# Optimization experiments

Hardware: AMD Instinct MI355X
Metric: run time of the kernel (lower is better)

## Reference

```python
import jax, jax.numpy as jnp
import numpy as np

N = 8192          # batch size (anchors == candidates, self-mining)
D = 128           # embedding dim
NUM_CLASSES = 256 # label vocabulary
MAX_K = 64        # static cap on negatives sampled per row (k ~= class_count-1 ~ 31)
MIN_DIST = 0.1
MAX_DIST = 1.42


def setup_inputs() -> dict:
    key = jax.random.key(0)
    k1, k2 = jax.random.split(key)
    l_embeds = jax.random.normal(k1, (N, D), dtype=jnp.float32)
    l_labels = jax.random.randint(k2, (N,), 0, NUM_CLASSES)
    return {"l_embeds": l_embeds, "l_labels": l_labels}


def reference(l_embeds, l_labels):
    # --- Miner.forward: L2-normalize embeddings (normalize_embeds=True) ---
    x = l_embeds / jnp.linalg.norm(l_embeds, axis=1, keepdims=True)

    # --- cdist(x, x, p=2) via gram matrix ---
    sq = jnp.sum(x * x, axis=1)                      # [N]
    d2 = sq[:, None] + sq[None, :] - 2.0 * (x @ x.T)  # [N, N]
    dist = jnp.sqrt(jnp.clip(d2, 0.0))

    # Exclude self-pairs: original adds inf on the diagonal; setting the diagonal
    # to MAX_DIST achieves the intended effect (zero weight via dist < max_dist)
    # without inf/nan propagation through log_weights.
    eye = jnp.eye(N, dtype=bool)
    dist = jnp.where(eye, MAX_DIST, dist)
    dist = jnp.clip(dist, MIN_DIST)

    neg = (l_labels[:, None] != l_labels[None, :]).astype(x.dtype)  # [N, N]

    # Distance-weighted sampling weights (inverse of q(d) on the hypersphere)
    d = float(D)
    log_weights = -((d - 2.0) * jnp.log(dist) + (d - 3.0) / 2.0 * (1.0 - dist * dist / 4.0))
    w = jnp.exp(log_weights - jnp.max(log_weights, axis=1, keepdims=True))
    w = w * neg * (dist < MAX_DIST).astype(x.dtype)
    w = w / jnp.clip(jnp.sum(w, axis=1, keepdims=True), 1e-6)  # row-normalized probs

    # Per-row number of negatives to sample: (# same-label rows) - 1 (self)
    counts = jnp.bincount(l_labels, length=NUM_CLASSES)
    k = counts[l_labels] - 1                                    # [N]

    # Vectorized weighted sampling WITH replacement (matches np.random.choice default):
    # categorical over log-probs, MAX_K draws per row, validity-masked to k draws.
    logits = jnp.where(w > 0, jnp.log(w), -1e30)
    keys = jax.random.split(jax.random.key(42), N)
    samples = jax.vmap(lambda kk, lg: jax.random.categorical(kk, lg, shape=(MAX_K,)))(keys, logits)  # [N, MAX_K]
    valid = jnp.arange(MAX_K)[None, :] < k[:, None]             # [N, MAX_K]
    rows = jnp.broadcast_to(jnp.arange(N)[:, None], (N, MAX_K))
    neg_mask = jnp.zeros((N, N), dtype=bool).at[rows, samples].max(valid)

    # Positive mask: same label, excluding self
    pos_mask = (l_labels[:, None] == l_labels[None, :]) & ~eye

    # Original returns nonzero() of pos_mask[:, :, None] & neg_mask[:, None, :]
    # (data-dependent shape); we return the dense masks + sampling weights,
    # from which the triplet index lists are trivially derived.
    return w, pos_mask, neg_mask
```

## Files before the change

### kernel.cpp

```cpp
#include <hip/hip_runtime.h>
#include <stdint.h>
#include <math.h>

#define NROWS 8192
#define DIM   128

__device__ __forceinline__ uint32_t rotl32(uint32_t x, int r) {
  return __builtin_amdgcn_alignbit(x, x, 32 - r);
}

__device__ __forceinline__ void threefry2x32(uint32_t k0, uint32_t k1,
                                             uint32_t x0, uint32_t x1,
                                             uint32_t& o0, uint32_t& o1) {
  uint32_t k2 = k0 ^ k1 ^ 0x1BD11BDAu;
  x0 += k0; x1 += k1;
#define TF4(a,b,c,d) \
  x0 += x1; x1 = rotl32(x1,a); x1 ^= x0; \
  x0 += x1; x1 = rotl32(x1,b); x1 ^= x0; \
  x0 += x1; x1 = rotl32(x1,c); x1 ^= x0; \
  x0 += x1; x1 = rotl32(x1,d); x1 ^= x0;
  TF4(13,15,26,6)
  x0 += k1; x1 += k2 + 1u;
  TF4(17,29,16,24)
  x0 += k2; x1 += k0 + 2u;
  TF4(13,15,26,6)
  x0 += k0; x1 += k1 + 3u;
  TF4(17,29,16,24)
  x0 += k1; x1 += k2 + 4u;
  TF4(13,15,26,6)
  x0 += k2; x1 += k0 + 5u;
#undef TF4
  o0 = x0; o1 = x1;
}

__global__ __launch_bounds__(256) void k_norm(const float* __restrict__ emb,
                                              float* __restrict__ xn,
                                              float* __restrict__ sq) {
  int row  = blockIdx.x * 4 + (threadIdx.x >> 6);
  int lane = threadIdx.x & 63;
  const float* r = emb + (size_t)row * DIM;
  float e0 = r[lane], e1 = r[lane + 64];
  float s = e0 * e0 + e1 * e1;
#pragma unroll
  for (int off = 32; off; off >>= 1) s += __shfl_xor(s, off);
  float nrm = sqrtf(s);
  float x0 = e0 / nrm, x1 = e1 / nrm;
  xn[(size_t)row * DIM + lane]      = x0;
  xn[(size_t)row * DIM + 64 + lane] = x1;
  float s2 = x0 * x0 + x1 * x1;
#pragma unroll
  for (int off = 32; off; off >>= 1) s2 += __shfl_xor(s2, off);
  if (lane == 0) sq[row] = s2;
}

__global__ void k_zero_counts(int* counts) { counts[threadIdx.x] = 0; }

__global__ void k_bincount(const int* __restrict__ lab, int* counts) {
  int i = blockIdx.x * blockDim.x + threadIdx.x;
  atomicAdd(&counts[lab[i]], 1);
}

__global__ void k_prep_rows(const int* __restrict__ lab, const int* __restrict__ counts,
                            int* __restrict__ kk, uint2* __restrict__ keys) {
  int i = blockIdx.x * blockDim.x + threadIdx.x;
  kk[i] = counts[lab[i]] - 1;
  uint32_t o0, o1;
  threefry2x32(0u, 42u, 0u, (uint32_t)i, o0, o1);
  keys[i] = make_uint2(o0, o1);
}

#define LSTR 68

__device__ __forceinline__ void tile_dots(const float* __restrict__ xn, int bi, int bj,
                                          float acc[4][4], float* As, float* Bs) {
  const int tid = threadIdx.x;
  const int ty = tid >> 4, tx = tid & 15;
#pragma unroll
  for (int r = 0; r < 4; ++r)
#pragma unroll
    for (int c = 0; c < 4; ++c) acc[r][c] = 0.0f;

  const int srow   = tid >> 4;
  const int schunk = tid & 15;
  for (int ks = 0; ks < DIM; ks += 64) {
    __syncthreads();
#pragma unroll
    for (int pr = 0; pr < 4; ++pr) {
      int rr = srow + pr * 16;
      float4 a4 = *(const float4*)(xn + (size_t)(bi * 64 + rr) * DIM + ks + schunk * 4);
      float4 b4 = *(const float4*)(xn + (size_t)(bj * 64 + rr) * DIM + ks + schunk * 4);
      int k0 = schunk * 4;
      As[(k0 + 0) * LSTR + rr] = a4.x; As[(k0 + 1) * LSTR + rr] = a4.y;
      As[(k0 + 2) * LSTR + rr] = a4.z; As[(k0 + 3) * LSTR + rr] = a4.w;
      Bs[(k0 + 0) * LSTR + rr] = b4.x; Bs[(k0 + 1) * LSTR + rr] = b4.y;
      Bs[(k0 + 2) * LSTR + rr] = b4.z; Bs[(k0 + 3) * LSTR + rr] = b4.w;
    }
    __syncthreads();
#pragma unroll 8
    for (int k = 0; k < 64; ++k) {
      float4 av = *(const float4*)(As + k * LSTR + ty * 4);
      float4 bv = *(const float4*)(Bs + k * LSTR + tx * 4);
      float a_[4] = {av.x, av.y, av.z, av.w};
      float b_[4] = {bv.x, bv.y, bv.z, bv.w};
#pragma unroll
      for (int r = 0; r < 4; ++r)
#pragma unroll
        for (int c = 0; c < 4; ++c)
          acc[r][c] = fmaf(a_[r], b_[c], acc[r][c]);
    }
  }
}

__global__ __launch_bounds__(256) void k_pass2(const float* __restrict__ xn,
                                               const float* __restrict__ sq,
                                               const int* __restrict__ lab,
                                               float* __restrict__ wout) {
  __shared__ float As[64 * LSTR];
  __shared__ float Bs[64 * LSTR];
  const int bi = blockIdx.y, bj = blockIdx.x;
  float acc[4][4];
  tile_dots(xn, bi, bj, acc, As, Bs);
  const int tid = threadIdx.x, ty = tid >> 4, tx = tid & 15;
  const int gi0 = bi * 64 + ty * 4, gj0 = bj * 64 + tx * 4;
  float sqi[4], sqj[4];
  int li[4], lj[4];
#pragma unroll
  for (int r = 0; r < 4; ++r) { sqi[r] = sq[gi0 + r]; li[r] = lab[gi0 + r]; }
#pragma unroll
  for (int c = 0; c < 4; ++c) { sqj[c] = sq[gj0 + c]; lj[c] = lab[gj0 + c]; }
#pragma unroll
  for (int r = 0; r < 4; ++r) {
    float tmp[4];
#pragma unroll
    for (int c = 0; c < 4; ++c) {
      float d2 = sqi[r] + sqj[c] - 2.0f * acc[r][c];
      float dist = sqrtf(fmaxf(d2, 0.0f));
      if (gi0 + r == gj0 + c) dist = 1.42f;
      dist = fmaxf(dist, 0.1f);
      float wun = 0.0f;
      if ((li[r] != lj[c]) && (dist < 1.42f)) {
        float logw = -(126.0f * logf(dist) + 62.5f * (1.0f - dist * dist * 0.25f));
        wun = expf(logw);
      }
      tmp[c] = wun;
    }
    float4 wv = {tmp[0], tmp[1], tmp[2], tmp[3]};
    *(float4*)(wout + (size_t)(gi0 + r) * NROWS + gj0) = wv;
  }
}

#define EPS_LAZY 1e-4f
#define ACAP 6400
#define NBINS 128
#define BININV 1.6f
#define GMAXF 15.95f
#define WGS 512
#define LOG2E 1.4426950408889634f

__global__ __launch_bounds__(WGS, 8) void k_sampler(const int* __restrict__ lab,
                                                    const int* __restrict__ kk,
                                                    const uint2* __restrict__ keys,
                                                    float* __restrict__ w,
                                                    float* __restrict__ pos,
                                                    float* __restrict__ neg) {
  __shared__ unsigned short act[ACAP + 64];
  __shared__ float wact[ACAP + 64];
  __shared__ int hist[NBINS];
  __shared__ float cmax[NBINS];
  __shared__ float redbuf[8];
  __shared__ float sbuf[4];
  __shared__ int acount;
  const int i = blockIdx.x;
  const int tid = threadIdx.x;
  const int wave = tid >> 6, lane = tid & 63;
  float* wrow   = w   + (size_t)i * NROWS;
  float* posrow = pos + (size_t)i * NROWS;
  float* negrow = neg + (size_t)i * NROWS;

  if (tid < 256) {
    float s0 = 0.0f;
    for (int c = tid; c < NROWS; c += 256) s0 += wrow[c];
#pragma unroll
    for (int off = 32; off; off >>= 1) s0 += __shfl_xor(s0, off);
    if ((tid & 63) == 0) sbuf[tid >> 6] = s0;
  }
  if (tid < NBINS) hist[tid] = 0;
  __syncthreads();
  const float s = (sbuf[0] + sbuf[1]) + (sbuf[2] + sbuf[3]);

  const int li = lab[i];
  float lmax = -3.4e38f;
  for (int c4 = tid * 4; c4 < NROWS; c4 += WGS * 4) {
    float4 wv = *(float4*)(wrow + c4);
    wv.x /= s; wv.y /= s; wv.z /= s; wv.w /= s;
    *(float4*)(wrow + c4) = wv;
    int4 lj = *(const int4*)(lab + c4);
    float4 pv;
    pv.x = (li == lj.x && (c4 + 0) != i) ? 1.0f : 0.0f;
    pv.y = (li == lj.y && (c4 + 1) != i) ? 1.0f : 0.0f;
    pv.z = (li == lj.z && (c4 + 2) != i) ? 1.0f : 0.0f;
    pv.w = (li == lj.w && (c4 + 3) != i) ? 1.0f : 0.0f;
    *(float4*)(posrow + c4) = pv;
    float4 z4 = {0.0f, 0.0f, 0.0f, 0.0f};
    *(float4*)(negrow + c4) = z4;
    float wa[4] = {wv.x, wv.y, wv.z, wv.w};
#pragma unroll
    for (int e = 0; e < 4; ++e) {
      if (wa[e] > 0.0f) {
        float l = logf(wa[e]);
        lmax = fmaxf(lmax, l);
        int bn = (int)(-l * BININV);
        bn = (bn < 0) ? 0 : ((bn > NBINS - 1) ? NBINS - 1 : bn);
        atomicAdd(&hist[bn], 1);
      }
    }
  }
#pragma unroll
  for (int off = 32; off; off >>= 1) lmax = fmaxf(lmax, __shfl_xor(lmax, off));
  if (lane == 0) redbuf[wave] = lmax;
  __syncthreads();

  const int kv = kk[i];
  if (kv <= 0) return;

  float gmax = redbuf[0];
#pragma unroll
  for (int rwv = 1; rwv < 8; ++rwv) gmax = fmaxf(gmax, redbuf[rwv]);
  float T = gmax - 20.43f;
  int bcut = (int)(-T * BININV);
  if (bcut > NBINS - 1) bcut = NBINS - 1;

  if (wave == 0) {
    int ex0 = 0, ex1 = 0, tot = 0;
    for (int k = 0; k < NBINS; ++k) {
      int h = (k <= bcut) ? hist[k] : 0;
      if (k < lane) ex0 += h;
      if (k < lane + 64) ex1 += h;
      tot += h;
    }
    hist[lane] = ex0;
    hist[lane + 64] = ex1;
    if (lane == 0) acount = tot;
  }
  __syncthreads();
  int A = acount;
  if (A > ACAP) A = ACAP;
  if (A == 0) return;

  for (int c = tid; c < NROWS; c += WGS) {
    float wv = wrow[c];
    if (wv > 0.0f) {
      float l = logf(wv);
      int bn = (int)(-l * BININV);
      bn = (bn < 0) ? 0 : ((bn > NBINS - 1) ? NBINS - 1 : bn);
      if (bn <= bcut) {
        int slot = atomicAdd(&hist[bn], 1);
        if (slot < ACAP) {
          act[slot] = (unsigned short)c;
          wact[slot] = wv;
        }
      }
    }
  }
  __syncthreads();
  if (tid < 64) { act[A + tid] = 0; wact[A + tid] = 0.0f; }
  __syncthreads();
  const int nch = (A + 63) >> 6;
  for (int j = wave; j < nch; j += 8) {
    float v = wact[(j << 6) + lane];
#pragma unroll
    for (int off = 32; off; off >>= 1) v = fmaxf(v, __shfl_xor(v, off));
    if (lane == 0) cmax[j] = logf(v);
  }
  __syncthreads();
  if (wave == 0) {
    float v1 = (lane + 64 < nch) ? cmax[lane + 64] : -3.4e38f;
    float v0 = (lane < nch) ? cmax[lane] : -3.4e38f;
#pragma unroll
    for (int off = 1; off < 64; off <<= 1) {
      float t1 = __shfl_down(v1, off); if (lane < 64 - off) v1 = fmaxf(v1, t1);
      float t0 = __shfl_down(v0, off); if (lane < 64 - off) v0 = fmaxf(v0, t0);
    }
    float h1max = __shfl(v1, 0);
    v0 = fmaxf(v0, h1max);
    if (lane < nch) cmax[lane] = v0;
    if (lane + 64 < nch) cmax[lane + 64] = v1;
  }
  __syncthreads();
  const uint2 key = keys[i];

  for (int t = 0; t < 8; ++t) {
    const int sN = wave + 8 * t;
    if (sN >= kv) break;
    const uint32_t sbase = (uint32_t)(sN * NROWS);
    float sbest = -3.4e38f;
    float nesl = -3.4e38f;
    int sidx = 0x7FFFFFFF;
    int j = 0;
    for (int base = 0; base < A; base += 64, ++j) {
      if (cmax[j] + GMAXF < sbest) break;
      int a = base + lane;
      int c = act[a];
      float wn = wact[a];
      uint32_t r0, r1;
      threefry2x32(key.x, key.y, 0u, sbase + (uint32_t)c, r0, r1);
      uint32_t b = (r0 ^ r1) >> 9;
      float bf = (float)b;
      float thr = fmaf(__builtin_amdgcn_exp2f(wn * nesl), 8388608.0f, -128.0f);
      if (__any(bf > thr)) {
        float u = b ? (bf * 1.1920928955078125e-7f) : 1.1754943508222875e-38f;
        float ge = -logf(-logf(u));
        float l = logf(wn);
        float ze = l + ge;
        int cc = c;
#pragma unroll
        for (int off = 1; off < 64; off <<= 1) {
          float oz = __shfl_xor(ze, off);
          int oc = __shfl_xor(cc, off);
          if (oz > ze || (oz == ze && oc < cc)) { ze = oz; cc = oc; }
        }
        if (ze > sbest || (ze == sbest && cc < sidx)) {
          sbest = ze; sidx = cc;
          nesl = -LOG2E * __expf(EPS_LAZY - sbest);
        }
      }
    }
    if (lane == 0) {
      negrow[sidx] = 1.0f;
    }
  }
}

extern "C" void kernel_launch(void* const* d_in, const int* in_sizes, int n_in,
                              void* d_out, int out_size, void* d_ws, size_t ws_size,
                              hipStream_t stream) {
  const float* emb = (const float*)d_in[0];
  const int* lab   = (const int*)d_in[1];
  float* out = (float*)d_out;
  const size_t NN = (size_t)NROWS * NROWS;
  float* w   = out;
  float* pos = out + NN;
  float* neg = out + 2 * NN;

  char* wsb = (char*)d_ws;
  float* xn     = (float*)(wsb);
  float* sq     = (float*)(wsb + 4194304);
  int*   kk     = (int*)  (wsb + 4194304 + 65536);
  uint2* keys   = (uint2*)(wsb + 4194304 + 98304);
  int*   counts = (int*)  (wsb + 4194304 + 163840);

  k_norm<<<NROWS / 4, 256, 0, stream>>>(emb, xn, sq);
  k_zero_counts<<<1, 256, 0, stream>>>(counts);
  k_bincount<<<NROWS / 256, 256, 0, stream>>>(lab, counts);
  k_prep_rows<<<NROWS / 256, 256, 0, stream>>>(lab, counts, kk, keys);
  dim3 g(NROWS / 64, NROWS / 64);
  k_pass2<<<g, 256, 0, stream>>>(xn, sq, lab, w);
  k_sampler<<<NROWS, WGS, 0, stream>>>(lab, kk, keys, w, pos, neg);
}
```

Before: 3.070 ms.

## Enlarge distance tiles to 128x128 and streamline Gumbel sampler with argmax seeding

The pairwise weight kernel now uses 128x128 output tiles with 8x8 per-thread register blocking, which raises arithmetic intensity per shared-memory load. The sampler packs column index and weight into one float2 array with a smaller capacity, drops the per-chunk max table and early break, and seeds each draw with the row's argmax column so the lazy threshold rejects most chunks from the start. Threefry is specialised so its first counter word is zero and it returns the folded XOR directly. Risks include register pressure from 64 accumulators, and losing the early exit, since every active chunk now hashes.

```diff
diff --git a/kernel.cpp b/kernel.cpp
--- a/kernel.cpp
+++ b/kernel.cpp
@@ -8,17 +8,18 @@
 __device__ __forceinline__ uint32_t rotl32(uint32_t x, int r) {
   return __builtin_amdgcn_alignbit(x, x, 32 - r);
 }
+
+#define TF4(a,b,c,d) \
+  x0 += x1; x1 = rotl32(x1,a); x1 ^= x0; \
+  x0 += x1; x1 = rotl32(x1,b); x1 ^= x0; \
+  x0 += x1; x1 = rotl32(x1,c); x1 ^= x0; \
+  x0 += x1; x1 = rotl32(x1,d); x1 ^= x0;
 
 __device__ __forceinline__ void threefry2x32(uint32_t k0, uint32_t k1,
                                              uint32_t x0, uint32_t x1,
                                              uint32_t& o0, uint32_t& o1) {
   uint32_t k2 = k0 ^ k1 ^ 0x1BD11BDAu;
   x0 += k0; x1 += k1;
-#define TF4(a,b,c,d) \
-  x0 += x1; x1 = rotl32(x1,a); x1 ^= x0; \
-  x0 += x1; x1 = rotl32(x1,b); x1 ^= x0; \
-  x0 += x1; x1 = rotl32(x1,c); x1 ^= x0; \
-  x0 += x1; x1 = rotl32(x1,d); x1 ^= x0;
   TF4(13,15,26,6)
   x0 += k1; x1 += k2 + 1u;
   TF4(17,29,16,24)
@@ -29,8 +30,24 @@
   x0 += k1; x1 += k2 + 4u;
   TF4(13,15,26,6)
   x0 += k2; x1 += k0 + 5u;
-#undef TF4
   o0 = x0; o1 = x1;
+}
+
+__device__ __forceinline__ uint32_t threefry_fold_prekeyed(uint32_t k0, uint32_t k1,
+                                                           uint32_t x1k) {
+  uint32_t k2 = k0 ^ k1 ^ 0x1BD11BDAu;
+  uint32_t x0 = k0, x1 = x1k;
+  TF4(13,15,26,6)
+  x0 += k1; x1 += k2 + 1u;
+  TF4(17,29,16,24)
+  x0 += k2; x1 += k0 + 2u;
+  TF4(13,15,26,6)
+  x0 += k0; x1 += k1 + 3u;
+  TF4(17,29,16,24)
+  x0 += k1; x1 += k2 + 4u;
+  TF4(13,15,26,6)
+  x0 += k2; x1 += k0 + 5u;
+  return x0 ^ x1;
 }
 
 __global__ __launch_bounds__(256) void k_norm(const float* __restrict__ emb,
@@ -69,91 +86,88 @@
   keys[i] = make_uint2(o0, o1);
 }
 
-#define LSTR 68
-
-__device__ __forceinline__ void tile_dots(const float* __restrict__ xn, int bi, int bj,
-                                          float acc[4][4], float* As, float* Bs) {
-  const int tid = threadIdx.x;
-  const int ty = tid >> 4, tx = tid & 15;
-#pragma unroll
-  for (int r = 0; r < 4; ++r)
-#pragma unroll
-    for (int c = 0; c < 4; ++c) acc[r][c] = 0.0f;
-
-  const int srow   = tid >> 4;
-  const int schunk = tid & 15;
-  for (int ks = 0; ks < DIM; ks += 64) {
-    __syncthreads();
-#pragma unroll
-    for (int pr = 0; pr < 4; ++pr) {
-      int rr = srow + pr * 16;
-      float4 a4 = *(const float4*)(xn + (size_t)(bi * 64 + rr) * DIM + ks + schunk * 4);
-      float4 b4 = *(const float4*)(xn + (size_t)(bj * 64 + rr) * DIM + ks + schunk * 4);
-      int k0 = schunk * 4;
-      As[(k0 + 0) * LSTR + rr] = a4.x; As[(k0 + 1) * LSTR + rr] = a4.y;
-      As[(k0 + 2) * LSTR + rr] = a4.z; As[(k0 + 3) * LSTR + rr] = a4.w;
-      Bs[(k0 + 0) * LSTR + rr] = b4.x; Bs[(k0 + 1) * LSTR + rr] = b4.y;
-      Bs[(k0 + 2) * LSTR + rr] = b4.z; Bs[(k0 + 3) * LSTR + rr] = b4.w;
-    }
-    __syncthreads();
-#pragma unroll 8
-    for (int k = 0; k < 64; ++k) {
-      float4 av = *(const float4*)(As + k * LSTR + ty * 4);
-      float4 bv = *(const float4*)(Bs + k * LSTR + tx * 4);
-      float a_[4] = {av.x, av.y, av.z, av.w};
-      float b_[4] = {bv.x, bv.y, bv.z, bv.w};
-#pragma unroll
-      for (int r = 0; r < 4; ++r)
-#pragma unroll
-        for (int c = 0; c < 4; ++c)
-          acc[r][c] = fmaf(a_[r], b_[c], acc[r][c]);
-    }
-  }
-}
+#define P2STR 132
 
 __global__ __launch_bounds__(256) void k_pass2(const float* __restrict__ xn,
                                                const float* __restrict__ sq,
                                                const int* __restrict__ lab,
                                                float* __restrict__ wout) {
-  __shared__ float As[64 * LSTR];
-  __shared__ float Bs[64 * LSTR];
+  __shared__ float As[32 * P2STR];
+  __shared__ float Bs[32 * P2STR];
   const int bi = blockIdx.y, bj = blockIdx.x;
-  float acc[4][4];
-  tile_dots(xn, bi, bj, acc, As, Bs);
-  const int tid = threadIdx.x, ty = tid >> 4, tx = tid & 15;
-  const int gi0 = bi * 64 + ty * 4, gj0 = bj * 64 + tx * 4;
-  float sqi[4], sqj[4];
-  int li[4], lj[4];
-#pragma unroll
-  for (int r = 0; r < 4; ++r) { sqi[r] = sq[gi0 + r]; li[r] = lab[gi0 + r]; }
-#pragma unroll
-  for (int c = 0; c < 4; ++c) { sqj[c] = sq[gj0 + c]; lj[c] = lab[gj0 + c]; }
-#pragma unroll
-  for (int r = 0; r < 4; ++r) {
-    float tmp[4];
-#pragma unroll
-    for (int c = 0; c < 4; ++c) {
+  const int tid = threadIdx.x;
+  const int ty = tid >> 4, tx = tid & 15;
+  float acc[8][8];
+#pragma unroll
+  for (int r = 0; r < 8; ++r)
+#pragma unroll
+    for (int c = 0; c < 8; ++c) acc[r][c] = 0.0f;
+
+  const int srow = tid >> 1;
+  const int sh   = (tid & 1) * 16;
+  for (int kc = 0; kc < DIM; kc += 32) {
+    __syncthreads();
+#pragma unroll
+    for (int q = 0; q < 4; ++q) {
+      int k0 = sh + q * 4;
+      float4 a4 = *(const float4*)(xn + (size_t)(bi * 128 + srow) * DIM + kc + k0);
+      float4 b4 = *(const float4*)(xn + (size_t)(bj * 128 + srow) * DIM + kc + k0);
+      As[(k0 + 0) * P2STR + srow] = a4.x; As[(k0 + 1) * P2STR + srow] = a4.y;
+      As[(k0 + 2) * P2STR + srow] = a4.z; As[(k0 + 3) * P2STR + srow] = a4.w;
+      Bs[(k0 + 0) * P2STR + srow] = b4.x; Bs[(k0 + 1) * P2STR + srow] = b4.y;
+      Bs[(k0 + 2) * P2STR + srow] = b4.z; Bs[(k0 + 3) * P2STR + srow] = b4.w;
+    }
+    __syncthreads();
+#pragma unroll 4
+    for (int k = 0; k < 32; ++k) {
+      float4 a0 = *(const float4*)(As + k * P2STR + ty * 8);
+      float4 a1 = *(const float4*)(As + k * P2STR + ty * 8 + 4);
+      float4 b0 = *(const float4*)(Bs + k * P2STR + tx * 8);
+      float4 b1 = *(const float4*)(Bs + k * P2STR + tx * 8 + 4);
+      float av[8] = {a0.x, a0.y, a0.z, a0.w, a1.x, a1.y, a1.z, a1.w};
+      float bv[8] = {b0.x, b0.y, b0.z, b0.w, b1.x, b1.y, b1.z, b1.w};
+#pragma unroll
+      for (int r = 0; r < 8; ++r)
+#pragma unroll
+        for (int c = 0; c < 8; ++c)
+          acc[r][c] = fmaf(av[r], bv[c], acc[r][c]);
+    }
+  }
+
+  const int gi0 = bi * 128 + ty * 8, gj0 = bj * 128 + tx * 8;
+  float sqi[8], sqj[8];
+  int li8[8], lj8[8];
+#pragma unroll
+  for (int r = 0; r < 8; ++r) { sqi[r] = sq[gi0 + r]; li8[r] = lab[gi0 + r]; }
+#pragma unroll
+  for (int c = 0; c < 8; ++c) { sqj[c] = sq[gj0 + c]; lj8[c] = lab[gj0 + c]; }
+#pragma unroll
+  for (int r = 0; r < 8; ++r) {
+    float tmp[8];
+#pragma unroll
+    for (int c = 0; c < 8; ++c) {
       float d2 = sqi[r] + sqj[c] - 2.0f * acc[r][c];
       float dist = sqrtf(fmaxf(d2, 0.0f));
       if (gi0 + r == gj0 + c) dist = 1.42f;
       dist = fmaxf(dist, 0.1f);
       float wun = 0.0f;
-      if ((li[r] != lj[c]) && (dist < 1.42f)) {
+      if ((li8[r] != lj8[c]) && (dist < 1.42f)) {
         float logw = -(126.0f * logf(dist) + 62.5f * (1.0f - dist * dist * 0.25f));
         wun = expf(logw);
       }
       tmp[c] = wun;
     }
-    float4 wv = {tmp[0], tmp[1], tmp[2], tmp[3]};
-    *(float4*)(wout + (size_t)(gi0 + r) * NROWS + gj0) = wv;
+    float4 w0 = {tmp[0], tmp[1], tmp[2], tmp[3]};
+    float4 w1 = {tmp[4], tmp[5], tmp[6], tmp[7]};
+    *(float4*)(wout + (size_t)(gi0 + r) * NROWS + gj0)     = w0;
+    *(float4*)(wout + (size_t)(gi0 + r) * NROWS + gj0 + 4) = w1;
   }
 }
 
 #define EPS_LAZY 1e-4f
-#define ACAP 6400
+#define ACAP 4608
 #define NBINS 128
 #define BININV 1.6f
-#define GMAXF 15.95f
 #define WGS 512
 #define LOG2E 1.4426950408889634f
 
@@ -163,11 +177,10 @@
                                                     float* __restrict__ w,
                                                     float* __restrict__ pos,
                                                     float* __restrict__ neg) {
-  __shared__ unsigned short act[ACAP + 64];
-  __shared__ float wact[ACAP + 64];
+  __shared__ float2 pact[ACAP + 64];
   __shared__ int hist[NBINS];
-  __shared__ float cmax[NBINS];
   __shared__ float redbuf[8];
+  __shared__ int redcol[8];
   __shared__ float sbuf[4];
   __shared__ int acount;
   const int i = blockIdx.x;
@@ -190,6 +203,7 @@
 
   const int li = lab[i];
   float lmax = -3.4e38f;
+  int lcol = 0x7FFFFFFF;
   for (int c4 = tid * 4; c4 < NROWS; c4 += WGS * 4) {
     float4 wv = *(float4*)(wrow + c4);
     wv.x /= s; wv.y /= s; wv.z /= s; wv.w /= s;
@@ -208,7 +222,7 @@
     for (int e = 0; e < 4; ++e) {
       if (wa[e] > 0.0f) {
         float l = logf(wa[e]);
-        lmax = fmaxf(lmax, l);
+        if (l > lmax) { lmax = l; lcol = c4 + e; }
         int bn = (int)(-l * BININV);
         bn = (bn < 0) ? 0 : ((bn > NBINS - 1) ? NBINS - 1 : bn);
         atomicAdd(&hist[bn], 1);
@@ -216,16 +230,24 @@
     }
   }
 #pragma unroll
-  for (int off = 32; off; off >>= 1) lmax = fmaxf(lmax, __shfl_xor(lmax, off));
-  if (lane == 0) redbuf[wave] = lmax;
+  for (int off = 32; off; off >>= 1) {
+    float ol = __shfl_xor(lmax, off);
+    int oc = __shfl_xor(lcol, off);
+    if (ol > lmax || (ol == lmax && oc < lcol)) { lmax = ol; lcol = oc; }
+  }
+  if (lane == 0) { redbuf[wave] = lmax; redcol[wave] = lcol; }
   __syncthreads();
 
   const int kv = kk[i];
   if (kv <= 0) return;
 
   float gmax = redbuf[0];
-#pragma unroll
-  for (int rwv = 1; rwv < 8; ++rwv) gmax = fmaxf(gmax, redbuf[rwv]);
+  int gcol = redcol[0];
+#pragma unroll
+  for (int rwv = 1; rwv < 8; ++rwv) {
+    float ol = redbuf[rwv]; int oc = redcol[rwv];
+    if (ol > gmax || (ol == gmax && oc < gcol)) { gmax = ol; gcol = oc; }
+  }
   float T = gmax - 20.43f;
   int bcut = (int)(-T * BININV);
   if (bcut > NBINS - 1) bcut = NBINS - 1;
@@ -256,55 +278,31 @@
       if (bn <= bcut) {
         int slot = atomicAdd(&hist[bn], 1);
         if (slot < ACAP) {
-          act[slot] = (unsigned short)c;
-          wact[slot] = wv;
+          pact[slot] = make_float2(wv, __uint_as_float((uint32_t)c));
         }
       }
     }
   }
   __syncthreads();
-  if (tid < 64) { act[A + tid] = 0; wact[A + tid] = 0.0f; }
-  __syncthreads();
-  const int nch = (A + 63) >> 6;
-  for (int j = wave; j < nch; j += 8) {
-    float v = wact[(j << 6) + lane];
-#pragma unroll
-    for (int off = 32; off; off >>= 1) v = fmaxf(v, __shfl_xor(v, off));
-    if (lane == 0) cmax[j] = logf(v);
-  }
-  __syncthreads();
-  if (wave == 0) {
-    float v1 = (lane + 64 < nch) ? cmax[lane + 64] : -3.4e38f;
-    float v0 = (lane < nch) ? cmax[lane] : -3.4e38f;
-#pragma unroll
-    for (int off = 1; off < 64; off <<= 1) {
-      float t1 = __shfl_down(v1, off); if (lane < 64 - off) v1 = fmaxf(v1, t1);
-      float t0 = __shfl_down(v0, off); if (lane < 64 - off) v0 = fmaxf(v0, t0);
-    }
-    float h1max = __shfl(v1, 0);
-    v0 = fmaxf(v0, h1max);
-    if (lane < nch) cmax[lane] = v0;
-    if (lane + 64 < nch) cmax[lane + 64] = v1;
-  }
+  if (tid < 64) pact[A + tid] = make_float2(0.0f, __uint_as_float(0u));
   __syncthreads();
   const uint2 key = keys[i];
 
   for (int t = 0; t < 8; ++t) {
     const int sN = wave + 8 * t;
     if (sN >= kv) break;
-    const uint32_t sbase = (uint32_t)(sN * NROWS);
-    float sbest = -3.4e38f;
-    float nesl = -3.4e38f;
-    int sidx = 0x7FFFFFFF;
-    int j = 0;
-    for (int base = 0; base < A; base += 64, ++j) {
-      if (cmax[j] + GMAXF < sbest) break;
-      int a = base + lane;
-      int c = act[a];
-      float wn = wact[a];
-      uint32_t r0, r1;
-      threefry2x32(key.x, key.y, 0u, sbase + (uint32_t)c, r0, r1);
-      uint32_t b = (r0 ^ r1) >> 9;
+    const uint32_t skey = (uint32_t)(sN * NROWS) + key.y;
+    uint32_t b0 = threefry_fold_prekeyed(key.x, key.y, (uint32_t)gcol + skey) >> 9;
+    float bf0 = (float)b0;
+    float u0 = b0 ? (bf0 * 1.1920928955078125e-7f) : 1.1754943508222875e-38f;
+    float sbest = gmax + (-logf(-logf(u0)));
+    int sidx = gcol;
+    float nesl = -LOG2E * __expf(EPS_LAZY - sbest);
+    for (int base = 0; base < A; base += 64) {
+      float2 p = pact[base + lane];
+      float wn = p.x;
+      uint32_t c = __float_as_uint(p.y);
+      uint32_t b = threefry_fold_prekeyed(key.x, key.y, c + skey) >> 9;
       float bf = (float)b;
       float thr = fmaf(__builtin_amdgcn_exp2f(wn * nesl), 8388608.0f, -128.0f);
       if (__any(bf > thr)) {
@@ -312,7 +310,7 @@
         float ge = -logf(-logf(u));
         float l = logf(wn);
         float ze = l + ge;
-        int cc = c;
+        int cc = (int)c;
 #pragma unroll
         for (int off = 1; off < 64; off <<= 1) {
           float oz = __shfl_xor(ze, off);
@@ -353,7 +351,7 @@
   k_zero_counts<<<1, 256, 0, stream>>>(counts);
   k_bincount<<<NROWS / 256, 256, 0, stream>>>(lab, counts);
   k_prep_rows<<<NROWS / 256, 256, 0, stream>>>(lab, counts, kk, keys);
-  dim3 g(NROWS / 64, NROWS / 64);
+  dim3 g(NROWS / 128, NROWS / 128);
   k_pass2<<<g, 256, 0, stream>>>(xn, sq, lab, w);
   k_sampler<<<NROWS, WGS, 0, stream>>>(lab, kk, keys, w, pos, neg);
 }
```

Result: slower. 3.237 ms (+5.4%).
